# Optimization experiments

Measured on AMD Instinct MI355X. Metric: run time of the kernel, lower is better.

Reference implementation:

```python
import jax, jax.numpy as jnp
import numpy as np

LP, LQ, B, IN, HID = 256, 256, 32, 512, 512
H = 2 * HID          # internal hidden size (hidden_size * 2)
IN2 = 2 * IN         # Up/Uq feature dim after self-concat
IN4 = 4 * IN


def setup_inputs() -> dict:
    key = jax.random.key(0)
    ks = jax.random.split(key, 12)
    def w(k, shape, fan):
        return (jax.random.normal(k, shape, jnp.float32) / np.float32(np.sqrt(fan)))
    return {
        "up": jax.random.normal(ks[0], (LP, B, IN), jnp.float32),
        "uq": jax.random.normal(ks[1], (LQ, B, IN), jnp.float32),
        "v0": jax.random.normal(ks[2], (B, H), jnp.float32),    # torch.randn v
        "Vvec": jax.random.normal(ks[3], (B, H), jnp.float32),  # torch.randn V (squeezed)
        "Wp": w(ks[4], (H, IN2), IN2),
        "Wq": w(ks[5], (H, IN2), IN2),
        "Wv": w(ks[6], (H, H), H),
        "Wg": w(ks[7], (IN4, IN4), IN4),
        "W_ih": w(ks[8], (3 * H, IN2), IN2),
        "W_hh": w(ks[9], (3 * H, H), H),
        "b_ih": w(ks[10], (3 * H,), H),
        "b_hh": w(ks[11], (3 * H,), H),
    }


def reference(up, uq, v0, Vvec, Wp, Wq, Wv, Wg, W_ih, W_hh, b_ih, b_hh):
    in2 = 2 * up.shape[2]
    # mixer indices are arange -> Up/Uq are just feature self-concats
    Up = jnp.concatenate([up, up], axis=2)   # [lp, B, in2]
    Uq = jnp.concatenate([uq, uq], axis=2)   # [lq, B, in2]
    # hoist loop-invariant projections (original recomputes Wq(Uq) each step)
    WUp = jnp.einsum('pbi,hi->pbh', Up, Wp)  # [lp, B, H]
    WUq = jnp.einsum('qbi,hi->qbh', Uq, Wq)  # [lq, B, H]

    def gru_cell(x, h):
        gi = x @ W_ih.T + b_ih
        gh = h @ W_hh.T + b_hh
        i_r, i_z, i_n = jnp.split(gi, 3, axis=1)
        h_r, h_z, h_n = jnp.split(gh, 3, axis=1)
        r = jax.nn.sigmoid(i_r + h_r)
        z = jax.nn.sigmoid(i_z + h_z)
        n = jnp.tanh(i_n + r * h_n)
        return (1.0 - z) * n + z * h

    def step(v, xs):
        up_i, wup_i = xs                                   # [B,in2], [B,H]
        x = jnp.tanh(wup_i[None] + WUq + (v @ Wv.T)[None])  # [lq, B, H]
        s = jnp.einsum('qbh,bh->bq', x, Vvec)               # [B, lq]
        a = jax.nn.softmax(s, axis=1)
        c = jnp.einsum('bq,qbd->bd', a, Uq)                 # [B, in2]
        r = jnp.concatenate([up_i, c], axis=1)              # [B, in4]
        g = jax.nn.sigmoid(r @ Wg.T)
        c_ = (g * r)[:, in2:]                               # gated context half
        v_new = gru_cell(c_, v)
        return v_new, v_new

    _, vs = jax.lax.scan(step, v0, (Up, WUp))   # vs: [lp, B, H]
    # dropout in eval mode = identity
    return vs
```

## Files before the change

### kernel.cpp

```cpp
#include <hip/hip_runtime.h>


#define NB 32
#define H 1024
#define H3 3072
#define LQn 256
#define LPn 256

__device__ __forceinline__ float fsig(float x) { return 1.0f / (1.0f + __expf(-x)); }
__device__ __forceinline__ float ftanh(float x) { return 1.0f - 2.0f / (1.0f + __expf(2.0f * x)); }

__global__ __launch_bounds__(256) void k_init(
    const float* __restrict__ v0, const float* __restrict__ Wp,
    const float* __restrict__ Wg, float* __restrict__ vbuf0,
    float* __restrict__ Wpf, float* __restrict__ Wg2f) {
  int i = blockIdx.x * 256 + threadIdx.x;
  if (i < NB * H) vbuf0[i] = v0[i];
  if (i < 1024 * 512) {
    int n = i >> 9, k = i & 511;
    Wpf[i] = Wp[(size_t)n * 1024 + k] + Wp[(size_t)n * 1024 + k + 512];
  }
  if (i < 1024 * 1024) {
    int j = i >> 10, kk = i & 1023;
    const float* wr = Wg + (size_t)(1024 + j) * 2048;
    Wg2f[i] = (kk < 512) ? (wr[kk] + wr[kk + 512]) : (wr[kk + 512] + wr[kk + 1024]);
  }
}

__global__ __launch_bounds__(256) void k_wuq(
    const float* __restrict__ A, const float* __restrict__ Wq, float* __restrict__ C) {
  __shared__ float As[16][65];
  __shared__ float Bs[16][65];
  int bm = blockIdx.x * 64, bn = blockIdx.y * 64;
  int t = threadIdx.x;
  int tx = t & 15, ty = t >> 4;
  float acc[4][4] = {};
  for (int k0 = 0; k0 < 512; k0 += 16) {
#pragma unroll
    for (int l = 0; l < 4; ++l) {
      int idx = t + l * 256;
      int row = idx >> 4, kk = idx & 15;
      As[kk][row] = A[(size_t)(bm + row) * 512 + k0 + kk];
      Bs[kk][row] = Wq[(size_t)(bn + row) * 1024 + k0 + kk] +
                    Wq[(size_t)(bn + row) * 1024 + k0 + kk + 512];
    }
    __syncthreads();
#pragma unroll
    for (int kk = 0; kk < 16; ++kk) {
      float a0[4], b0[4];
#pragma unroll
      for (int i = 0; i < 4; ++i) a0[i] = As[kk][ty * 4 + i];
#pragma unroll
      for (int j = 0; j < 4; ++j) b0[j] = Bs[kk][tx * 4 + j];
#pragma unroll
      for (int i = 0; i < 4; ++i)
#pragma unroll
        for (int j = 0; j < 4; ++j) acc[i][j] += a0[i] * b0[j];
    }
    __syncthreads();
  }
#pragma unroll
  for (int i = 0; i < 4; ++i)
#pragma unroll
    for (int j = 0; j < 4; ++j)
      C[(size_t)(bm + ty * 4 + i) * 1024 + bn + tx * 4 + j] = acc[i][j];
}

__global__ __launch_bounds__(256, 1) void k_A(
    const float* __restrict__ gi, const float* __restrict__ gh_old,
    const float* __restrict__ v_old, const float* __restrict__ up,
    const float* __restrict__ Wv, const float* __restrict__ W_hh,
    const float* __restrict__ b_hh, const float* __restrict__ Wpf,
    float* __restrict__ v_new_g, float* __restrict__ out,
    float* __restrict__ t_out, float* __restrict__ gh_new, int p) {
  int s = blockIdx.x & 63, bg = blockIdx.x >> 6;
  int b0 = bg * 8;
  int tid = threadIdx.x, lane = tid & 63, wave = tid >> 6;
  __shared__ float vnew[8][H];
  __shared__ float upb[8][512];

  if (p == 0) {
    for (int bb = 0; bb < 8; ++bb)
#pragma unroll
      for (int ii = 0; ii < 4; ++ii) {
        int h = tid + ii * 256;
        vnew[bb][h] = v_old[(size_t)(b0 + bb) * H + h];
      }
  } else {
    for (int bb = 0; bb < 8; ++bb) {
      int b = b0 + bb;
      const float* gib = gi + (size_t)b * H3;
      const float* ghb = gh_old + (size_t)b * H3;
#pragma unroll
      for (int ii = 0; ii < 4; ++ii) {
        int h = tid + ii * 256;
        float rg = fsig(gib[h] + ghb[h]);
        float z = fsig(gib[H + h] + ghb[H + h]);
        float nn = ftanh(gib[2 * H + h] + rg * ghb[2 * H + h]);
        float vo = v_old[(size_t)b * H + h];
        float vn = (1.0f - z) * nn + z * vo;
        vnew[bb][h] = vn;
        if (s == 0) {
          v_new_g[(size_t)b * H + h] = vn;
          out[((size_t)(p - 1) * NB + b) * H + h] = vn;
        }
      }
    }
  }
  bool is_t = (s < 16);
  if (is_t) {
    for (int idx = tid; idx < 8 * 512; idx += 256) {
      int bb = idx >> 9, k = idx & 511;
      upb[bb][k] = up[((size_t)p * NB + (b0 + bb)) * 512 + k];
    }
  }
  __syncthreads();

  float vreg[8][16];
#pragma unroll
  for (int bb = 0; bb < 8; ++bb)
#pragma unroll
    for (int i = 0; i < 16; ++i) vreg[bb][i] = vnew[bb][lane + i * 64];

  int n0 = s * 64 + wave * 16;
  for (int rr = 0; rr < 16; ++rr) {
    int n = n0 + rr;
    float acc[8];
#pragma unroll
    for (int bb = 0; bb < 8; ++bb) acc[bb] = 0.0f;
    if (is_t) {
      const float* wr = Wv + (size_t)n * H;
#pragma unroll
      for (int i = 0; i < 16; ++i) {
        float w = wr[lane + i * 64];
#pragma unroll
        for (int bb = 0; bb < 8; ++bb) acc[bb] = fmaf(w, vreg[bb][i], acc[bb]);
      }
      const float* wp = Wpf + (size_t)n * 512;
#pragma unroll
      for (int i = 0; i < 8; ++i) {
        float w = wp[lane + i * 64];
#pragma unroll
        for (int bb = 0; bb < 8; ++bb) acc[bb] = fmaf(w, upb[bb][lane + i * 64], acc[bb]);
      }
#pragma unroll
      for (int bb = 0; bb < 8; ++bb) {
        float a = acc[bb];
#pragma unroll
        for (int o = 32; o >= 1; o >>= 1) a += __shfl_xor(a, o, 64);
        if (lane == 0) t_out[(size_t)(b0 + bb) * H + n] = a;
      }
    } else {
      int m = n - H;
      const float* wr = W_hh + (size_t)m * H;
#pragma unroll
      for (int i = 0; i < 16; ++i) {
        float w = wr[lane + i * 64];
#pragma unroll
        for (int bb = 0; bb < 8; ++bb) acc[bb] = fmaf(w, vreg[bb][i], acc[bb]);
      }
      float bias = b_hh[m];
#pragma unroll
      for (int bb = 0; bb < 8; ++bb) {
        float a = acc[bb];
#pragma unroll
        for (int o = 32; o >= 1; o >>= 1) a += __shfl_xor(a, o, 64);
        if (lane == 0) gh_new[(size_t)(b0 + bb) * H3 + m] = a + bias;
      }
    }
  }
}

__global__ __launch_bounds__(64) void k_B(
    const float* __restrict__ t_in, const float* __restrict__ WUq,
    const float* __restrict__ Vvec, float* __restrict__ s_out) {
  int q = blockIdx.x >> 5, b = blockIdx.x & 31;
  int lane = threadIdx.x;
  const float* wq = WUq + ((size_t)q * NB + b) * H;
  const float* tb = t_in + (size_t)b * H;
  const float* vv = Vvec + (size_t)b * H;
  float a = 0.0f;
#pragma unroll
  for (int i = 0; i < 16; ++i) {
    int h = lane + i * 64;
    a += ftanh(tb[h] + wq[h]) * vv[h];
  }
#pragma unroll
  for (int o = 32; o >= 1; o >>= 1) a += __shfl_xor(a, o, 64);
  if (lane == 0) s_out[b * LQn + q] = a;
}

__global__ __launch_bounds__(256) void k_C(
    const float* __restrict__ s_in, const float* __restrict__ uq,
    const float* __restrict__ up, float* __restrict__ rhalf, int p) {
  int b = blockIdx.x;
  int tid = threadIdx.x, lane = tid & 63, wave = tid >> 6;
  __shared__ float a_s[256];
  __shared__ float red[4];
  float sv = s_in[b * LQn + tid];
  float m = sv;
#pragma unroll
  for (int o = 32; o >= 1; o >>= 1) m = fmaxf(m, __shfl_xor(m, o, 64));
  if (lane == 0) red[wave] = m;
  __syncthreads();
  float bm = fmaxf(fmaxf(red[0], red[1]), fmaxf(red[2], red[3]));
  __syncthreads();
  float e = __expf(sv - bm);
  float se = e;
#pragma unroll
  for (int o = 32; o >= 1; o >>= 1) se += __shfl_xor(se, o, 64);
  if (lane == 0) red[wave] = se;
  __syncthreads();
  float tot = red[0] + red[1] + red[2] + red[3];
  a_s[tid] = e / tot;
  __syncthreads();
  rhalf[(size_t)b * 1024 + tid] = up[((size_t)p * NB + b) * 512 + tid];
  rhalf[(size_t)b * 1024 + tid + 256] = up[((size_t)p * NB + b) * 512 + tid + 256];
  float acc0 = 0.0f, acc1 = 0.0f;
  for (int q = 0; q < LQn; ++q) {
    float a = a_s[q];
    const float* uqr = uq + ((size_t)q * NB + b) * 512;
    acc0 += a * uqr[tid];
    acc1 += a * uqr[tid + 256];
  }
  rhalf[(size_t)b * 1024 + 512 + tid] = acc0;
  rhalf[(size_t)b * 1024 + 512 + tid + 256] = acc1;
}

__global__ __launch_bounds__(256, 1) void k_D(
    const float* __restrict__ rhalf, const float* __restrict__ Wg2f,
    float* __restrict__ c_g) {
  int s = blockIdx.x & 63, bg = blockIdx.x >> 6, b0 = bg * 8;
  int tid = threadIdx.x, lane = tid & 63, wave = tid >> 6;
  float rreg[8][16];
#pragma unroll
  for (int bb = 0; bb < 8; ++bb)
#pragma unroll
    for (int i = 0; i < 16; ++i)
      rreg[bb][i] = rhalf[(size_t)(b0 + bb) * 1024 + lane + i * 64];
  int j0 = s * 16 + wave * 4;
  for (int rr = 0; rr < 4; ++rr) {
    int j = j0 + rr;
    const float* wr = Wg2f + (size_t)j * 1024;
    float acc[8];
#pragma unroll
    for (int bb = 0; bb < 8; ++bb) acc[bb] = 0.0f;
#pragma unroll
    for (int i = 0; i < 16; ++i) {
      float w = wr[lane + i * 64];
#pragma unroll
      for (int bb = 0; bb < 8; ++bb) acc[bb] = fmaf(w, rreg[bb][i], acc[bb]);
    }
#pragma unroll
    for (int bb = 0; bb < 8; ++bb) {
      float a = acc[bb];
#pragma unroll
      for (int o = 32; o >= 1; o >>= 1) a += __shfl_xor(a, o, 64);
      if (lane == 0) {
        float cv = rhalf[(size_t)(b0 + bb) * 1024 + 512 + (j & 511)];
        c_g[(size_t)(b0 + bb) * 1024 + j] = fsig(a) * cv;
      }
    }
  }
}

__global__ __launch_bounds__(256, 1) void k_E(
    const float* __restrict__ c_g, const float* __restrict__ W_ih,
    const float* __restrict__ b_ih, float* __restrict__ gi) {
  int s = blockIdx.x & 63, bg = blockIdx.x >> 6, b0 = bg * 8;
  int tid = threadIdx.x, lane = tid & 63, wave = tid >> 6;
  float creg[8][16];
#pragma unroll
  for (int bb = 0; bb < 8; ++bb)
#pragma unroll
    for (int i = 0; i < 16; ++i)
      creg[bb][i] = c_g[(size_t)(b0 + bb) * 1024 + lane + i * 64];
  int r0 = s * 48 + wave * 12;
  for (int rr = 0; rr < 12; ++rr) {
    int r = r0 + rr;
    const float* wr = W_ih + (size_t)r * 1024;
    float acc[8];
#pragma unroll
    for (int bb = 0; bb < 8; ++bb) acc[bb] = 0.0f;
#pragma unroll
    for (int i = 0; i < 16; ++i) {
      float w = wr[lane + i * 64];
#pragma unroll
      for (int bb = 0; bb < 8; ++bb) acc[bb] = fmaf(w, creg[bb][i], acc[bb]);
    }
    float bias = b_ih[r];
#pragma unroll
    for (int bb = 0; bb < 8; ++bb) {
      float a = acc[bb];
#pragma unroll
      for (int o = 32; o >= 1; o >>= 1) a += __shfl_xor(a, o, 64);
      if (lane == 0) gi[(size_t)(b0 + bb) * H3 + r] = a + bias;
    }
  }
}

__global__ __launch_bounds__(256) void k_fin(
    const float* __restrict__ gi, const float* __restrict__ gh_old,
    const float* __restrict__ v_old, float* __restrict__ out) {
  int i = blockIdx.x * 256 + threadIdx.x;
  int b = i >> 10, h = i & 1023;
  const float* gib = gi + (size_t)b * H3;
  const float* ghb = gh_old + (size_t)b * H3;
  float rg = fsig(gib[h] + ghb[h]);
  float z = fsig(gib[H + h] + ghb[H + h]);
  float nn = ftanh(gib[2 * H + h] + rg * ghb[2 * H + h]);
  float vn = (1.0f - z) * nn + z * v_old[i];
  out[(size_t)255 * NB * H + i] = vn;
}

extern "C" void kernel_launch(void* const* d_in, const int* in_sizes, int n_in,
                              void* d_out, int out_size, void* d_ws, size_t ws_size,
                              hipStream_t stream) {
  const float* up = (const float*)d_in[0];
  const float* uq = (const float*)d_in[1];
  const float* v0 = (const float*)d_in[2];
  const float* Vvec = (const float*)d_in[3];
  const float* Wp = (const float*)d_in[4];
  const float* Wq = (const float*)d_in[5];
  const float* Wv = (const float*)d_in[6];
  const float* Wg = (const float*)d_in[7];
  const float* W_ih = (const float*)d_in[8];
  const float* W_hh = (const float*)d_in[9];
  const float* b_ih = (const float*)d_in[10];
  const float* b_hh = (const float*)d_in[11];
  float* out = (float*)d_out;
  float* ws = (float*)d_ws;

  float* vbuf0 = ws;
  float* vbuf1 = ws + 32768;
  float* tbuf  = ws + 65536;
  float* gh0   = ws + 98304;
  float* gh1   = ws + 196608;
  float* sbuf  = ws + 294912;
  float* rhalf = ws + 303104;
  float* cbuf  = ws + 335872;
  float* gibuf = ws + 368640;
  float* Wpf   = ws + 466944;
  float* Wg2f  = ws + 991232;
  float* WUq   = ws + 2039808;

  k_init<<<4096, 256, 0, stream>>>(v0, Wp, Wg, vbuf0, Wpf, Wg2f);
  k_wuq<<<dim3(128, 16), 256, 0, stream>>>(uq, Wq, WUq);

  for (int p = 0; p < 256; ++p) {
    float* ghn = (p & 1) ? gh1 : gh0;
    float* gho = (p & 1) ? gh0 : gh1;
    float* vn = (p & 1) ? vbuf1 : vbuf0;
    float* vo = (p & 1) ? vbuf0 : vbuf1;
    if (p == 0) { vo = vbuf0; vn = vbuf1; }
    k_A<<<256, 256, 0, stream>>>(gibuf, gho, vo, up, Wv, W_hh, b_hh, Wpf,
                                 vn, out, tbuf, ghn, p);
    k_B<<<8192, 64, 0, stream>>>(tbuf, WUq, Vvec, sbuf);
    k_C<<<32, 256, 0, stream>>>(sbuf, uq, up, rhalf, p);
    k_D<<<256, 256, 0, stream>>>(rhalf, Wg2f, cbuf);
    k_E<<<256, 256, 0, stream>>>(cbuf, W_ih, b_ih, gibuf);
  }
  k_fin<<<128, 256, 0, stream>>>(gibuf, gh1, vbuf1, out);
}
```

Baseline: 29.70 ms.

## Fuse per-step kernels into one persistent kernel with grid barriers

Replaces the 5 kernel launches per timestep (1280 total) with a single persistent 256-block kernel that loops over all timesteps and separates stages with atomic-counter grid barriers. The hidden state now stays in shared memory across steps instead of round-tripping through global buffers. The softmax-context stage is spread over all 256 blocks using atomicAdd instead of 32 blocks. It assumes all 256 blocks are co-resident, and each step now pays for five global barriers.

```diff
diff --git a/kernel.cpp b/kernel.cpp
--- a/kernel.cpp
+++ b/kernel.cpp
@@ -5,17 +5,27 @@
 #define H 1024
 #define H3 3072
 #define LQn 256
-#define LPn 256
 
 __device__ __forceinline__ float fsig(float x) { return 1.0f / (1.0f + __expf(-x)); }
 __device__ __forceinline__ float ftanh(float x) { return 1.0f - 2.0f / (1.0f + __expf(2.0f * x)); }
 
+__device__ __forceinline__ void gbar(unsigned* __restrict__ ctr, int id) {
+  __syncthreads();
+  if (threadIdx.x == 0) {
+    __threadfence();
+    __hip_atomic_fetch_add(&ctr[id], 1u, __ATOMIC_RELAXED, __HIP_MEMORY_SCOPE_AGENT);
+    while (__hip_atomic_load(&ctr[id], __ATOMIC_RELAXED, __HIP_MEMORY_SCOPE_AGENT) < 256u) {
+      __builtin_amdgcn_s_sleep(2);
+    }
+    __threadfence();
+  }
+  __syncthreads();
+}
+
 __global__ __launch_bounds__(256) void k_init(
-    const float* __restrict__ v0, const float* __restrict__ Wp,
-    const float* __restrict__ Wg, float* __restrict__ vbuf0,
+    const float* __restrict__ Wp, const float* __restrict__ Wg,
     float* __restrict__ Wpf, float* __restrict__ Wg2f) {
   int i = blockIdx.x * 256 + threadIdx.x;
-  if (i < NB * H) vbuf0[i] = v0[i];
   if (i < 1024 * 512) {
     int n = i >> 9, k = i & 511;
     Wpf[i] = Wp[(size_t)n * 1024 + k] + Wp[(size_t)n * 1024 + k + 512];
@@ -25,6 +35,11 @@
     const float* wr = Wg + (size_t)(1024 + j) * 2048;
     Wg2f[i] = (kk < 512) ? (wr[kk] + wr[kk + 512]) : (wr[kk + 512] + wr[kk + 1024]);
   }
+}
+
+__global__ __launch_bounds__(256) void k_zero(unsigned* __restrict__ ctr) {
+  int i = blockIdx.x * 256 + threadIdx.x;
+  if (i < 2048) ctr[i] = 0u;
 }
 
 __global__ __launch_bounds__(256) void k_wuq(
@@ -66,251 +81,265 @@
       C[(size_t)(bm + ty * 4 + i) * 1024 + bn + tx * 4 + j] = acc[i][j];
 }
 
-__global__ __launch_bounds__(256, 1) void k_A(
-    const float* __restrict__ gi, const float* __restrict__ gh_old,
-    const float* __restrict__ v_old, const float* __restrict__ up,
+__global__ __launch_bounds__(256, 1) void k_scan(
+    const float* __restrict__ up, const float* __restrict__ uq,
+    const float* __restrict__ v0, const float* __restrict__ Vvec,
     const float* __restrict__ Wv, const float* __restrict__ W_hh,
-    const float* __restrict__ b_hh, const float* __restrict__ Wpf,
-    float* __restrict__ v_new_g, float* __restrict__ out,
-    float* __restrict__ t_out, float* __restrict__ gh_new, int p) {
-  int s = blockIdx.x & 63, bg = blockIdx.x >> 6;
-  int b0 = bg * 8;
-  int tid = threadIdx.x, lane = tid & 63, wave = tid >> 6;
+    const float* __restrict__ b_hh, const float* __restrict__ W_ih,
+    const float* __restrict__ b_ih, const float* __restrict__ Wpf,
+    const float* __restrict__ Wg2f, const float* __restrict__ WUq,
+    float* __restrict__ tbuf, float* __restrict__ gh0, float* __restrict__ gh1,
+    float* __restrict__ sbuf, float* __restrict__ rhalf, float* __restrict__ cbuf,
+    float* __restrict__ gibuf, float* __restrict__ out, unsigned* __restrict__ ctr) {
+  const int blk = blockIdx.x, tid = threadIdx.x;
+  const int lane = tid & 63, wave = tid >> 6;
+  const int s = blk & 63, bg = blk >> 6, b0 = bg * 8;
   __shared__ float vnew[8][H];
   __shared__ float upb[8][512];
-
-  if (p == 0) {
-    for (int bb = 0; bb < 8; ++bb)
-#pragma unroll
-      for (int ii = 0; ii < 4; ++ii) {
-        int h = tid + ii * 256;
-        vnew[bb][h] = v_old[(size_t)(b0 + bb) * H + h];
-      }
-  } else {
-    for (int bb = 0; bb < 8; ++bb) {
-      int b = b0 + bb;
-      const float* gib = gi + (size_t)b * H3;
-      const float* ghb = gh_old + (size_t)b * H3;
-#pragma unroll
-      for (int ii = 0; ii < 4; ++ii) {
-        int h = tid + ii * 256;
-        float rg = fsig(gib[h] + ghb[h]);
-        float z = fsig(gib[H + h] + ghb[H + h]);
-        float nn = ftanh(gib[2 * H + h] + rg * ghb[2 * H + h]);
-        float vo = v_old[(size_t)b * H + h];
-        float vn = (1.0f - z) * nn + z * vo;
-        vnew[bb][h] = vn;
-        if (s == 0) {
-          v_new_g[(size_t)b * H + h] = vn;
-          out[((size_t)(p - 1) * NB + b) * H + h] = vn;
-        }
-      }
-    }
-  }
-  bool is_t = (s < 16);
-  if (is_t) {
-    for (int idx = tid; idx < 8 * 512; idx += 256) {
-      int bb = idx >> 9, k = idx & 511;
-      upb[bb][k] = up[((size_t)p * NB + (b0 + bb)) * 512 + k];
-    }
-  }
-  __syncthreads();
-
-  float vreg[8][16];
-#pragma unroll
-  for (int bb = 0; bb < 8; ++bb)
-#pragma unroll
-    for (int i = 0; i < 16; ++i) vreg[bb][i] = vnew[bb][lane + i * 64];
-
-  int n0 = s * 64 + wave * 16;
-  for (int rr = 0; rr < 16; ++rr) {
-    int n = n0 + rr;
-    float acc[8];
-#pragma unroll
-    for (int bb = 0; bb < 8; ++bb) acc[bb] = 0.0f;
-    if (is_t) {
-      const float* wr = Wv + (size_t)n * H;
-#pragma unroll
-      for (int i = 0; i < 16; ++i) {
-        float w = wr[lane + i * 64];
-#pragma unroll
-        for (int bb = 0; bb < 8; ++bb) acc[bb] = fmaf(w, vreg[bb][i], acc[bb]);
-      }
-      const float* wp = Wpf + (size_t)n * 512;
-#pragma unroll
-      for (int i = 0; i < 8; ++i) {
-        float w = wp[lane + i * 64];
-#pragma unroll
-        for (int bb = 0; bb < 8; ++bb) acc[bb] = fmaf(w, upb[bb][lane + i * 64], acc[bb]);
-      }
-#pragma unroll
-      for (int bb = 0; bb < 8; ++bb) {
-        float a = acc[bb];
-#pragma unroll
-        for (int o = 32; o >= 1; o >>= 1) a += __shfl_xor(a, o, 64);
-        if (lane == 0) t_out[(size_t)(b0 + bb) * H + n] = a;
-      }
-    } else {
-      int m = n - H;
-      const float* wr = W_hh + (size_t)m * H;
-#pragma unroll
-      for (int i = 0; i < 16; ++i) {
-        float w = wr[lane + i * 64];
-#pragma unroll
-        for (int bb = 0; bb < 8; ++bb) acc[bb] = fmaf(w, vreg[bb][i], acc[bb]);
-      }
-      float bias = b_hh[m];
-#pragma unroll
-      for (int bb = 0; bb < 8; ++bb) {
-        float a = acc[bb];
-#pragma unroll
-        for (int o = 32; o >= 1; o >>= 1) a += __shfl_xor(a, o, 64);
-        if (lane == 0) gh_new[(size_t)(b0 + bb) * H3 + m] = a + bias;
-      }
-    }
-  }
-}
-
-__global__ __launch_bounds__(64) void k_B(
-    const float* __restrict__ t_in, const float* __restrict__ WUq,
-    const float* __restrict__ Vvec, float* __restrict__ s_out) {
-  int q = blockIdx.x >> 5, b = blockIdx.x & 31;
-  int lane = threadIdx.x;
-  const float* wq = WUq + ((size_t)q * NB + b) * H;
-  const float* tb = t_in + (size_t)b * H;
-  const float* vv = Vvec + (size_t)b * H;
-  float a = 0.0f;
-#pragma unroll
-  for (int i = 0; i < 16; ++i) {
-    int h = lane + i * 64;
-    a += ftanh(tb[h] + wq[h]) * vv[h];
-  }
-#pragma unroll
-  for (int o = 32; o >= 1; o >>= 1) a += __shfl_xor(a, o, 64);
-  if (lane == 0) s_out[b * LQn + q] = a;
-}
-
-__global__ __launch_bounds__(256) void k_C(
-    const float* __restrict__ s_in, const float* __restrict__ uq,
-    const float* __restrict__ up, float* __restrict__ rhalf, int p) {
-  int b = blockIdx.x;
-  int tid = threadIdx.x, lane = tid & 63, wave = tid >> 6;
   __shared__ float a_s[256];
   __shared__ float red[4];
-  float sv = s_in[b * LQn + tid];
-  float m = sv;
-#pragma unroll
-  for (int o = 32; o >= 1; o >>= 1) m = fmaxf(m, __shfl_xor(m, o, 64));
-  if (lane == 0) red[wave] = m;
-  __syncthreads();
-  float bm = fmaxf(fmaxf(red[0], red[1]), fmaxf(red[2], red[3]));
-  __syncthreads();
-  float e = __expf(sv - bm);
-  float se = e;
-#pragma unroll
-  for (int o = 32; o >= 1; o >>= 1) se += __shfl_xor(se, o, 64);
-  if (lane == 0) red[wave] = se;
-  __syncthreads();
-  float tot = red[0] + red[1] + red[2] + red[3];
-  a_s[tid] = e / tot;
-  __syncthreads();
-  rhalf[(size_t)b * 1024 + tid] = up[((size_t)p * NB + b) * 512 + tid];
-  rhalf[(size_t)b * 1024 + tid + 256] = up[((size_t)p * NB + b) * 512 + tid + 256];
-  float acc0 = 0.0f, acc1 = 0.0f;
-  for (int q = 0; q < LQn; ++q) {
-    float a = a_s[q];
-    const float* uqr = uq + ((size_t)q * NB + b) * 512;
-    acc0 += a * uqr[tid];
-    acc1 += a * uqr[tid + 256];
-  }
-  rhalf[(size_t)b * 1024 + 512 + tid] = acc0;
-  rhalf[(size_t)b * 1024 + 512 + tid + 256] = acc1;
-}
-
-__global__ __launch_bounds__(256, 1) void k_D(
-    const float* __restrict__ rhalf, const float* __restrict__ Wg2f,
-    float* __restrict__ c_g) {
-  int s = blockIdx.x & 63, bg = blockIdx.x >> 6, b0 = bg * 8;
-  int tid = threadIdx.x, lane = tid & 63, wave = tid >> 6;
-  float rreg[8][16];
-#pragma unroll
-  for (int bb = 0; bb < 8; ++bb)
-#pragma unroll
-    for (int i = 0; i < 16; ++i)
-      rreg[bb][i] = rhalf[(size_t)(b0 + bb) * 1024 + lane + i * 64];
-  int j0 = s * 16 + wave * 4;
-  for (int rr = 0; rr < 4; ++rr) {
-    int j = j0 + rr;
-    const float* wr = Wg2f + (size_t)j * 1024;
-    float acc[8];
-#pragma unroll
-    for (int bb = 0; bb < 8; ++bb) acc[bb] = 0.0f;
-#pragma unroll
-    for (int i = 0; i < 16; ++i) {
-      float w = wr[lane + i * 64];
-#pragma unroll
-      for (int bb = 0; bb < 8; ++bb) acc[bb] = fmaf(w, rreg[bb][i], acc[bb]);
-    }
-#pragma unroll
-    for (int bb = 0; bb < 8; ++bb) {
-      float a = acc[bb];
-#pragma unroll
-      for (int o = 32; o >= 1; o >>= 1) a += __shfl_xor(a, o, 64);
-      if (lane == 0) {
-        float cv = rhalf[(size_t)(b0 + bb) * 1024 + 512 + (j & 511)];
-        c_g[(size_t)(b0 + bb) * 1024 + j] = fsig(a) * cv;
-      }
-    }
-  }
-}
-
-__global__ __launch_bounds__(256, 1) void k_E(
-    const float* __restrict__ c_g, const float* __restrict__ W_ih,
-    const float* __restrict__ b_ih, float* __restrict__ gi) {
-  int s = blockIdx.x & 63, bg = blockIdx.x >> 6, b0 = bg * 8;
-  int tid = threadIdx.x, lane = tid & 63, wave = tid >> 6;
-  float creg[8][16];
-#pragma unroll
-  for (int bb = 0; bb < 8; ++bb)
-#pragma unroll
-    for (int i = 0; i < 16; ++i)
-      creg[bb][i] = c_g[(size_t)(b0 + bb) * 1024 + lane + i * 64];
-  int r0 = s * 48 + wave * 12;
-  for (int rr = 0; rr < 12; ++rr) {
-    int r = r0 + rr;
-    const float* wr = W_ih + (size_t)r * 1024;
-    float acc[8];
-#pragma unroll
-    for (int bb = 0; bb < 8; ++bb) acc[bb] = 0.0f;
-#pragma unroll
-    for (int i = 0; i < 16; ++i) {
-      float w = wr[lane + i * 64];
-#pragma unroll
-      for (int bb = 0; bb < 8; ++bb) acc[bb] = fmaf(w, creg[bb][i], acc[bb]);
-    }
-    float bias = b_ih[r];
-#pragma unroll
-    for (int bb = 0; bb < 8; ++bb) {
-      float a = acc[bb];
-#pragma unroll
-      for (int o = 32; o >= 1; o >>= 1) a += __shfl_xor(a, o, 64);
-      if (lane == 0) gi[(size_t)(b0 + bb) * H3 + r] = a + bias;
-    }
-  }
-}
-
-__global__ __launch_bounds__(256) void k_fin(
-    const float* __restrict__ gi, const float* __restrict__ gh_old,
-    const float* __restrict__ v_old, float* __restrict__ out) {
-  int i = blockIdx.x * 256 + threadIdx.x;
-  int b = i >> 10, h = i & 1023;
-  const float* gib = gi + (size_t)b * H3;
-  const float* ghb = gh_old + (size_t)b * H3;
-  float rg = fsig(gib[h] + ghb[h]);
-  float z = fsig(gib[H + h] + ghb[H + h]);
-  float nn = ftanh(gib[2 * H + h] + rg * ghb[2 * H + h]);
-  float vn = (1.0f - z) * nn + z * v_old[i];
-  out[(size_t)255 * NB * H + i] = vn;
+
+  for (int p = 0; p < 256; ++p) {
+    float* ghn = (p & 1) ? gh1 : gh0;
+    float* gho = (p & 1) ? gh0 : gh1;
+    const int bid = p * 5;
+
+    if (p == 0) {
+      for (int bb = 0; bb < 8; ++bb)
+#pragma unroll
+        for (int ii = 0; ii < 4; ++ii) {
+          int h = tid + ii * 256;
+          vnew[bb][h] = v0[(size_t)(b0 + bb) * H + h];
+        }
+    } else {
+      for (int bb = 0; bb < 8; ++bb) {
+        int b = b0 + bb;
+        const float* gib = gibuf + (size_t)b * H3;
+        const float* ghb = gho + (size_t)b * H3;
+#pragma unroll
+        for (int ii = 0; ii < 4; ++ii) {
+          int h = tid + ii * 256;
+          float rg = fsig(gib[h] + ghb[h]);
+          float z = fsig(gib[H + h] + ghb[H + h]);
+          float nn = ftanh(gib[2 * H + h] + rg * ghb[2 * H + h]);
+          float vn = (1.0f - z) * nn + z * vnew[bb][h];
+          vnew[bb][h] = vn;
+          if (s == 0) out[((size_t)(p - 1) * NB + b) * H + h] = vn;
+        }
+      }
+    }
+    const bool is_t = (s < 16);
+    if (is_t) {
+      for (int idx = tid; idx < 8 * 512; idx += 256) {
+        int bb = idx >> 9, k = idx & 511;
+        upb[bb][k] = up[((size_t)p * NB + (b0 + bb)) * 512 + k];
+      }
+    }
+    __syncthreads();
+
+    {
+      float vreg[8][16];
+#pragma unroll
+      for (int bb = 0; bb < 8; ++bb)
+#pragma unroll
+        for (int i = 0; i < 16; ++i) vreg[bb][i] = vnew[bb][lane + i * 64];
+
+      int n0 = s * 64 + wave * 16;
+      for (int rr = 0; rr < 16; ++rr) {
+        int n = n0 + rr;
+        float acc[8];
+#pragma unroll
+        for (int bb = 0; bb < 8; ++bb) acc[bb] = 0.0f;
+        if (is_t) {
+          const float* wr = Wv + (size_t)n * H;
+#pragma unroll
+          for (int i = 0; i < 16; ++i) {
+            float w = wr[lane + i * 64];
+#pragma unroll
+            for (int bb = 0; bb < 8; ++bb) acc[bb] = fmaf(w, vreg[bb][i], acc[bb]);
+          }
+          const float* wp = Wpf + (size_t)n * 512;
+#pragma unroll
+          for (int i = 0; i < 8; ++i) {
+            float w = wp[lane + i * 64];
+#pragma unroll
+            for (int bb = 0; bb < 8; ++bb) acc[bb] = fmaf(w, upb[bb][lane + i * 64], acc[bb]);
+          }
+#pragma unroll
+          for (int bb = 0; bb < 8; ++bb) {
+            float a = acc[bb];
+#pragma unroll
+            for (int o = 32; o >= 1; o >>= 1) a += __shfl_xor(a, o, 64);
+            if (lane == 0) tbuf[(size_t)(b0 + bb) * H + n] = a;
+          }
+        } else {
+          int m = n - H;
+          const float* wr = W_hh + (size_t)m * H;
+#pragma unroll
+          for (int i = 0; i < 16; ++i) {
+            float w = wr[lane + i * 64];
+#pragma unroll
+            for (int bb = 0; bb < 8; ++bb) acc[bb] = fmaf(w, vreg[bb][i], acc[bb]);
+          }
+          float bias = b_hh[m];
+#pragma unroll
+          for (int bb = 0; bb < 8; ++bb) {
+            float a = acc[bb];
+#pragma unroll
+            for (int o = 32; o >= 1; o >>= 1) a += __shfl_xor(a, o, 64);
+            if (lane == 0) ghn[(size_t)(b0 + bb) * H3 + m] = a + bias;
+          }
+        }
+      }
+    }
+    gbar(ctr, bid + 0);
+
+    {
+      if (blk < NB) {
+        int b = blk;
+        float* rb = rhalf + (size_t)b * 1024;
+        const float* ub = up + ((size_t)p * NB + b) * 512;
+        rb[tid] = ub[tid];
+        rb[tid + 256] = ub[tid + 256];
+        rb[512 + tid] = 0.0f;
+        rb[768 + tid] = 0.0f;
+      }
+      int q = blk;
+      const float* wqb = WUq + (size_t)q * NB * H;
+      for (int r = 0; r < 8; ++r) {
+        int b = wave * 8 + r;
+        const float* wq = wqb + (size_t)b * H;
+        const float* tb = tbuf + (size_t)b * H;
+        const float* vv = Vvec + (size_t)b * H;
+        float a = 0.0f;
+#pragma unroll
+        for (int i = 0; i < 16; ++i) {
+          int h = lane + i * 64;
+          a += ftanh(tb[h] + wq[h]) * vv[h];
+        }
+#pragma unroll
+        for (int o = 32; o >= 1; o >>= 1) a += __shfl_xor(a, o, 64);
+        if (lane == 0) sbuf[b * LQn + q] = a;
+      }
+    }
+    gbar(ctr, bid + 1);
+
+    {
+      int b = blk & 31, qs = blk >> 5;
+      float sv = sbuf[b * LQn + tid];
+      float m = sv;
+#pragma unroll
+      for (int o = 32; o >= 1; o >>= 1) m = fmaxf(m, __shfl_xor(m, o, 64));
+      if (lane == 0) red[wave] = m;
+      __syncthreads();
+      float bm = fmaxf(fmaxf(red[0], red[1]), fmaxf(red[2], red[3]));
+      __syncthreads();
+      float e = __expf(sv - bm);
+      float se = e;
+#pragma unroll
+      for (int o = 32; o >= 1; o >>= 1) se += __shfl_xor(se, o, 64);
+      if (lane == 0) red[wave] = se;
+      __syncthreads();
+      float tot = red[0] + red[1] + red[2] + red[3];
+      a_s[tid] = e / tot;
+      __syncthreads();
+      int q0 = qs * 32;
+      float acc0 = 0.0f, acc1 = 0.0f;
+#pragma unroll 8
+      for (int qq = 0; qq < 32; ++qq) {
+        float a = a_s[q0 + qq];
+        const float* uqr = uq + ((size_t)(q0 + qq) * NB + b) * 512;
+        acc0 = fmaf(a, uqr[tid], acc0);
+        acc1 = fmaf(a, uqr[tid + 256], acc1);
+      }
+      atomicAdd(&rhalf[(size_t)b * 1024 + 512 + tid], acc0);
+      atomicAdd(&rhalf[(size_t)b * 1024 + 768 + tid], acc1);
+    }
+    gbar(ctr, bid + 2);
+
+    {
+      float rreg[16];
+      int j0 = s * 16 + wave * 4;
+      float accs[4][8];
+#pragma unroll
+      for (int rr = 0; rr < 4; ++rr)
+#pragma unroll
+        for (int bb = 0; bb < 8; ++bb) accs[rr][bb] = 0.0f;
+      for (int bb = 0; bb < 8; ++bb) {
+#pragma unroll
+        for (int i = 0; i < 16; ++i)
+          rreg[i] = rhalf[(size_t)(b0 + bb) * 1024 + lane + i * 64];
+#pragma unroll
+        for (int rr = 0; rr < 4; ++rr) {
+          const float* wr = Wg2f + (size_t)(j0 + rr) * 1024;
+          float a = 0.0f;
+#pragma unroll
+          for (int i = 0; i < 16; ++i) a = fmaf(wr[lane + i * 64], rreg[i], a);
+          accs[rr][bb] = a;
+        }
+      }
+#pragma unroll
+      for (int rr = 0; rr < 4; ++rr) {
+        int j = j0 + rr;
+#pragma unroll
+        for (int bb = 0; bb < 8; ++bb) {
+          float a = accs[rr][bb];
+#pragma unroll
+          for (int o = 32; o >= 1; o >>= 1) a += __shfl_xor(a, o, 64);
+          if (lane == 0) {
+            float cv = rhalf[(size_t)(b0 + bb) * 1024 + 512 + (j & 511)];
+            cbuf[(size_t)(b0 + bb) * 1024 + j] = fsig(a) * cv;
+          }
+        }
+      }
+    }
+    gbar(ctr, bid + 3);
+
+    {
+      float creg[8][16];
+#pragma unroll
+      for (int bb = 0; bb < 8; ++bb)
+#pragma unroll
+        for (int i = 0; i < 16; ++i)
+          creg[bb][i] = cbuf[(size_t)(b0 + bb) * 1024 + lane + i * 64];
+      int r0 = s * 48 + wave * 12;
+      for (int rr = 0; rr < 12; ++rr) {
+        int r = r0 + rr;
+        const float* wr = W_ih + (size_t)r * 1024;
+        float acc[8];
+#pragma unroll
+        for (int bb = 0; bb < 8; ++bb) acc[bb] = 0.0f;
+#pragma unroll
+        for (int i = 0; i < 16; ++i) {
+          float w = wr[lane + i * 64];
+#pragma unroll
+          for (int bb = 0; bb < 8; ++bb) acc[bb] = fmaf(w, creg[bb][i], acc[bb]);
+        }
+        float bias = b_ih[r];
+#pragma unroll
+        for (int bb = 0; bb < 8; ++bb) {
+          float a = acc[bb];
+#pragma unroll
+          for (int o = 32; o >= 1; o >>= 1) a += __shfl_xor(a, o, 64);
+          if (lane == 0) gibuf[(size_t)(b0 + bb) * H3 + r] = a + bias;
+        }
+      }
+    }
+    gbar(ctr, bid + 4);
+  }
+
+  if (tid < 128) {
+    int bb = tid >> 4;
+    int h = s * 16 + (tid & 15);
+    int b = b0 + bb;
+    const float* gib = gibuf + (size_t)b * H3;
+    const float* ghb = gh1 + (size_t)b * H3;
+    float rg = fsig(gib[h] + ghb[h]);
+    float z = fsig(gib[H + h] + ghb[H + h]);
+    float nn = ftanh(gib[2 * H + h] + rg * ghb[2 * H + h]);
+    float vn = (1.0f - z) * nn + z * vnew[bb][h];
+    out[((size_t)255 * NB + b) * H + h] = vn;
+  }
 }
 
 extern "C" void kernel_launch(void* const* d_in, const int* in_sizes, int n_in,
@@ -331,34 +360,22 @@
   float* out = (float*)d_out;
   float* ws = (float*)d_ws;
 
-  float* vbuf0 = ws;
-  float* vbuf1 = ws + 32768;
-  float* tbuf  = ws + 65536;
-  float* gh0   = ws + 98304;
-  float* gh1   = ws + 196608;
-  float* sbuf  = ws + 294912;
-  float* rhalf = ws + 303104;
-  float* cbuf  = ws + 335872;
-  float* gibuf = ws + 368640;
-  float* Wpf   = ws + 466944;
-  float* Wg2f  = ws + 991232;
-  float* WUq   = ws + 2039808;
-
-  k_init<<<4096, 256, 0, stream>>>(v0, Wp, Wg, vbuf0, Wpf, Wg2f);
+  float* tbuf = ws;
+  float* gh0 = ws + 32768;
+  float* gh1 = ws + 131072;
+  float* sbuf = ws + 229376;
+  float* rhalf = ws + 237568;
+  float* cbuf = ws + 270336;
+  float* gibuf = ws + 303104;
+  float* Wpf = ws + 401408;
+  float* Wg2f = ws + 925696;
+  float* WUq = ws + 1974272;
+  unsigned* ctr = (unsigned*)(ws + 10362880);
+
+  k_init<<<4096, 256, 0, stream>>>(Wp, Wg, Wpf, Wg2f);
+  k_zero<<<8, 256, 0, stream>>>(ctr);
   k_wuq<<<dim3(128, 16), 256, 0, stream>>>(uq, Wq, WUq);
-
-  for (int p = 0; p < 256; ++p) {
-    float* ghn = (p & 1) ? gh1 : gh0;
-    float* gho = (p & 1) ? gh0 : gh1;
-    float* vn = (p & 1) ? vbuf1 : vbuf0;
-    float* vo = (p & 1) ? vbuf0 : vbuf1;
-    if (p == 0) { vo = vbuf0; vn = vbuf1; }
-    k_A<<<256, 256, 0, stream>>>(gibuf, gho, vo, up, Wv, W_hh, b_hh, Wpf,
-                                 vn, out, tbuf, ghn, p);
-    k_B<<<8192, 64, 0, stream>>>(tbuf, WUq, Vvec, sbuf);
-    k_C<<<32, 256, 0, stream>>>(sbuf, uq, up, rhalf, p);
-    k_D<<<256, 256, 0, stream>>>(rhalf, Wg2f, cbuf);
-    k_E<<<256, 256, 0, stream>>>(cbuf, W_ih, b_ih, gibuf);
-  }
-  k_fin<<<128, 256, 0, stream>>>(gibuf, gh1, vbuf1, out);
-}
+  k_scan<<<256, 256, 0, stream>>>(up, uq, v0, Vvec, Wv, W_hh, b_hh, W_ih, b_ih,
+                                  Wpf, Wg2f, WUq, tbuf, gh0, gh1, sbuf, rhalf,
+                                  cbuf, gibuf, out, ctr);
+}
```

Measured after the change: 73.35 ms. +146.9%, slower.
